# Kernel tuning notes

Measured on AMD Instinct MI355X. Metric: run time of the kernel, lower is better.

Reference implementation:

```python
import jax, jax.numpy as jnp
import numpy as np

N_VERTICES = 1_000_000
N_EDGES = 16_000_000


def setup_inputs() -> dict:
    key = jax.random.key(0)
    k1, k2, k3 = jax.random.split(key, 3)
    vertex_attr = jax.random.normal(k1, (N_VERTICES, 2), dtype=jnp.float32)
    edgeij_pair = jax.random.randint(k2, (2, N_EDGES), 0, N_VERTICES, dtype=jnp.int64)
    edge_attr = jax.random.normal(k3, (N_EDGES, 2), dtype=jnp.float32)
    g = jnp.zeros((1, 1), dtype=jnp.float32)
    batch = jnp.zeros((N_VERTICES,), dtype=jnp.int64)
    return {"vertex_attr": vertex_attr, "edgeij_pair": edgeij_pair,
            "edge_attr": edge_attr, "g": g, "batch": batch}


def reference(vertex_attr, edgeij_pair, edge_attr, g, batch):
    # c_ij: second edge feature column, [E, 1]
    c_ij = edge_attr[:, 1:2]
    b_i = vertex_attr[:, 0:1]  # [N, 1]
    x_i = vertex_attr[:, 1:2]  # [N, 1]
    n_vertices = x_i.shape[0]
    # edge-to-vertex aggregation: sum c_ij into receiving vertex i (row 0)
    cbar_i = jax.ops.segment_sum(c_ij, edgeij_pair[0], num_segments=n_vertices)
    r_i = b_i - cbar_i
    return jnp.concatenate([b_i, x_i, r_i], axis=1)  # [N, 3]
```

## Files before the change

kernel.cpp:

```cpp
#include <hip/hip_runtime.h>


#define BSHIFT 11
#define BSIZE (1 << BSHIFT)
#define NBUCK_PAD 512
#define TILE 8192
#define TPB 1024
#define PGRID 512

#define BARL() do { \
    asm volatile("s_waitcnt lgkmcnt(0)" ::: "memory"); \
    __builtin_amdgcn_s_barrier(); } while (0)

__global__ __launch_bounds__(TPB, 8)
void vu_partition(const int* __restrict__ src,
                  const float* __restrict__ eattr,
                  unsigned long long* __restrict__ pairs,
                  unsigned int* __restrict__ alloc,
                  int ne, int nbuck, int cap) {
    __shared__ unsigned long long sorted[TILE];
    __shared__ unsigned int hist[NBUCK_PAD];
    __shared__ unsigned int base_l[NBUCK_PAD];
    __shared__ unsigned int cursor[NBUCK_PAD];
    __shared__ unsigned int gbase[NBUCK_PAD];
    __shared__ unsigned int wsum[8];
    __shared__ unsigned int wexcl[8];

    const int t = threadIdx.x;
    const int nt_tiles = (ne + TILE - 1) / TILE;

    int   s0, s1, s2, s3, s4, s5, s6, s7;
    float c0, c1, c2, c3, c4, c5, c6, c7;

    int tk = blockIdx.x;

    if (tk < nt_tiles) {
        int tile0 = tk * TILE;
        if (tile0 + TILE <= ne) {
            const int* sp = src + tile0 + t;
            const float* cp = eattr + 2 * (tile0 + t) + 1;
            s0 = sp[0 * 1024]; s1 = sp[1 * 1024];
            s2 = sp[2 * 1024]; s3 = sp[3 * 1024];
            s4 = sp[4 * 1024]; s5 = sp[5 * 1024];
            s6 = sp[6 * 1024]; s7 = sp[7 * 1024];
            c0 = cp[0 * 2048]; c1 = cp[1 * 2048];
            c2 = cp[2 * 2048]; c3 = cp[3 * 2048];
            c4 = cp[4 * 2048]; c5 = cp[5 * 2048];
            c6 = cp[6 * 2048]; c7 = cp[7 * 2048];
        }
    }
    if (t < NBUCK_PAD) hist[t] = 0u;
    BARL();

    for (; tk < nt_tiles; tk += PGRID) {
        int tile0 = tk * TILE;
        int lim = ne - tile0; if (lim > TILE) lim = TILE;
        bool full = (lim == TILE);

        int nk = tk + PGRID;
        bool pv = (nk < nt_tiles) && (nk * TILE + TILE <= ne);
        int   p0s, p1s, p2s, p3s, p4s, p5s, p6s, p7s;
        float p0c, p1c, p2c, p3c, p4c, p5c, p6c, p7c;
        if (pv) {
            int ptile0 = nk * TILE;
            const int* sp = src + ptile0 + t;
            const float* cp = eattr + 2 * (ptile0 + t) + 1;
            p0s = sp[0 * 1024]; p1s = sp[1 * 1024];
            p2s = sp[2 * 1024]; p3s = sp[3 * 1024];
            p4s = sp[4 * 1024]; p5s = sp[5 * 1024];
            p6s = sp[6 * 1024]; p7s = sp[7 * 1024];
            p0c = cp[0 * 2048]; p1c = cp[1 * 2048];
            p2c = cp[2 * 2048]; p3c = cp[3 * 2048];
            p4c = cp[4 * 2048]; p5c = cp[5 * 2048];
            p6c = cp[6 * 2048]; p7c = cp[7 * 2048];
        }

        if (full) {
            atomicAdd(&hist[((unsigned)s0) >> BSHIFT], 1u);
            atomicAdd(&hist[((unsigned)s1) >> BSHIFT], 1u);
            atomicAdd(&hist[((unsigned)s2) >> BSHIFT], 1u);
            atomicAdd(&hist[((unsigned)s3) >> BSHIFT], 1u);
            atomicAdd(&hist[((unsigned)s4) >> BSHIFT], 1u);
            atomicAdd(&hist[((unsigned)s5) >> BSHIFT], 1u);
            atomicAdd(&hist[((unsigned)s6) >> BSHIFT], 1u);
            atomicAdd(&hist[((unsigned)s7) >> BSHIFT], 1u);
        } else {
            for (int i = t; i < lim; i += TPB)
                atomicAdd(&hist[((unsigned)src[tile0 + i]) >> BSHIFT], 1u);
        }
        BARL();

        unsigned int mycnt = (t < NBUCK_PAD) ? hist[t] : 0u;
        if (t < NBUCK_PAD) hist[t] = 0u;
        unsigned int gb = 0u;
        if (t < nbuck && mycnt) gb = atomicAdd(&alloc[t], mycnt);

        unsigned int x = mycnt;
        #pragma unroll
        for (int off = 1; off < 64; off <<= 1) {
            unsigned int v = __shfl_up(x, off, 64);
            if ((t & 63) >= off) x += v;
        }
        if (t < NBUCK_PAD && (t & 63) == 63) wsum[t >> 6] = x;
        BARL();
        if (t < 8) {
            unsigned int s = 0u;
            for (int k = 0; k < t; ++k) s += wsum[k];
            wexcl[t] = s;
        }
        BARL();
        if (t < NBUCK_PAD) {
            unsigned int excl = x + wexcl[t >> 6] - mycnt;
            base_l[t] = excl;
            cursor[t] = excl;
            gbase[t] = gb;
        }
        BARL();

#define VU_SCAT(sv, cv) do { \
        unsigned int q_ = ((unsigned)(sv)) >> BSHIFT; \
        unsigned int pos_ = atomicAdd(&cursor[q_], 1u); \
        sorted[pos_] = ((unsigned long long)__float_as_uint(cv) << 32) \
                       | (unsigned)(sv); } while (0)
        if (full) {
            VU_SCAT(s0, c0); VU_SCAT(s1, c1);
            VU_SCAT(s2, c2); VU_SCAT(s3, c3);
            VU_SCAT(s4, c4); VU_SCAT(s5, c5);
            VU_SCAT(s6, c6); VU_SCAT(s7, c7);
        } else {
            for (int i = t; i < lim; i += TPB) {
                int e = tile0 + i;
                int s = src[e];
                float2 ec = ((const float2*)eattr)[e];
                VU_SCAT(s, ec.y);
            }
        }
#undef VU_SCAT
        BARL();

        for (int i = t; i < lim; i += TPB) {
            unsigned long long p = sorted[i];
            unsigned int q = ((unsigned int)p) >> BSHIFT;
            unsigned int dst = q * (unsigned int)cap + gbase[q]
                             + ((unsigned int)i - base_l[q]);
            unsigned int hi = q * (unsigned int)cap + (unsigned int)cap - 1u;
            if (dst > hi) dst = hi;
            pairs[dst] = p;
        }

        s0 = p0s; s1 = p1s; s2 = p2s; s3 = p3s;
        s4 = p4s; s5 = p5s; s6 = p6s; s7 = p7s;
        c0 = p0c; c1 = p1c; c2 = p2c; c3 = p3c;
        c4 = p4c; c5 = p5c; c6 = p6c; c7 = p7c;
    }
}

__global__ __launch_bounds__(1024)
void vu_aggregate(const unsigned long long* __restrict__ pairs,
                  const unsigned int* __restrict__ alloc,
                  const float* __restrict__ vattr,
                  float* __restrict__ out,
                  int nv, int cap) {
    __shared__ float acc[BSIZE];
    __shared__ float obuf[BSIZE * 3];
    int q = blockIdx.x;
    int t = threadIdx.x;
    acc[t] = 0.0f;
    acc[t + 1024] = 0.0f;

    int v0 = q << BSHIFT;
    int iv0 = v0 + t, iv1 = v0 + t + 1024;
    float2 va0 = make_float2(0.f, 0.f), va1 = make_float2(0.f, 0.f);
    if (iv0 < nv) va0 = ((const float2*)vattr)[iv0];
    if (iv1 < nv) va1 = ((const float2*)vattr)[iv1];
    __syncthreads();

    unsigned int cnt = alloc[q];
    if (cnt > (unsigned int)cap) cnt = (unsigned int)cap;
    const unsigned long long* p = pairs + (size_t)q * (size_t)cap;
    const ulonglong2* p2 = (const ulonglong2*)p;
    unsigned int n2 = cnt >> 1;

#define VU_ACC(v64) do { \
        atomicAdd(&acc[((unsigned int)(v64)) & (BSIZE - 1)], \
                  __uint_as_float((unsigned int)((v64) >> 32))); } while (0)

    unsigned int i = t;
    for (; i + 3u * 1024u < n2; i += 4096u) {
        ulonglong2 v0 = p2[i];
        ulonglong2 v1 = p2[i + 1024u];
        ulonglong2 v2 = p2[i + 2048u];
        ulonglong2 v3 = p2[i + 3072u];
        VU_ACC(v0.x); VU_ACC(v0.y);
        VU_ACC(v1.x); VU_ACC(v1.y);
        VU_ACC(v2.x); VU_ACC(v2.y);
        VU_ACC(v3.x); VU_ACC(v3.y);
    }
    for (; i < n2; i += 1024u) {
        ulonglong2 v = p2[i];
        VU_ACC(v.x); VU_ACC(v.y);
    }
    if (t == 0 && (cnt & 1u)) {
        unsigned long long v = p[cnt - 1];
        VU_ACC(v);
    }
#undef VU_ACC
    __syncthreads();

    if (iv0 < nv) {
        obuf[3 * t + 0] = va0.x;
        obuf[3 * t + 1] = va0.y;
        obuf[3 * t + 2] = va0.x - acc[t];
    }
    {
        int i2 = t + 1024;
        if (iv1 < nv) {
            obuf[3 * i2 + 0] = va1.x;
            obuf[3 * i2 + 1] = va1.y;
            obuf[3 * i2 + 2] = va1.x - acc[i2];
        }
    }
    __syncthreads();

    long fbase = (long)q * (BSIZE * 3);
    int nfl = 3 * nv - (int)fbase;
    if (nfl > BSIZE * 3) nfl = BSIZE * 3;
    if (nfl > 0) {
        float4* o4 = (float4*)(out + fbase);
        const float4* s4 = (const float4*)obuf;
        int n4 = nfl >> 2;
        for (int j = t; j < n4; j += 1024) o4[j] = s4[j];
        for (int j = (n4 << 2) + t; j < nfl; j += 1024) out[fbase + j] = obuf[j];
    }
}

__global__ void vu_init_kernel(const float* __restrict__ vattr,
                               float* __restrict__ out, int n) {
    int i = blockIdx.x * blockDim.x + threadIdx.x;
    if (i < n) {
        float2 v = ((const float2*)vattr)[i];
        out[3 * i + 0] = v.x;
        out[3 * i + 1] = v.y;
        out[3 * i + 2] = v.x;
    }
}

__global__ void vu_scatter_kernel(const int* __restrict__ src,
                                  const float* __restrict__ eattr,
                                  float* __restrict__ out, int ne) {
    int t = blockIdx.x * blockDim.x + threadIdx.x;
    int e0 = t * 4;
    if (e0 + 3 < ne) {
        int4 idx = ((const int4*)src)[t];
        float4 a = ((const float4*)eattr)[2 * t + 0];
        float4 b = ((const float4*)eattr)[2 * t + 1];
        atomicAdd(&out[3 * idx.x + 2], -a.y);
        atomicAdd(&out[3 * idx.y + 2], -a.w);
        atomicAdd(&out[3 * idx.z + 2], -b.y);
        atomicAdd(&out[3 * idx.w + 2], -b.w);
    } else {
        for (int e = e0; e < ne; ++e)
            atomicAdd(&out[3 * src[e] + 2], -eattr[2 * e + 1]);
    }
}

extern "C" void kernel_launch(void* const* d_in, const int* in_sizes, int n_in,
                              void* d_out, int out_size, void* d_ws, size_t ws_size,
                              hipStream_t stream) {
    const float* vattr = (const float*)d_in[0];
    const int* edges = (const int*)d_in[1];
    const float* eattr = (const float*)d_in[2];
    float* out = (float*)d_out;

    int nv = in_sizes[0] / 2;
    int ne = in_sizes[2] / 2;

    int nbuck = (nv + BSIZE - 1) >> BSHIFT;
    int mean = ne / nbuck;
    int cap = mean + mean / 8 + 1024;
    cap = (cap + 15) & ~15;

    size_t alloc_bytes = 4096;
    size_t pair_bytes = (size_t)nbuck * (size_t)cap * 8ull;
    size_t need = alloc_bytes + pair_bytes;

    if (ws_size >= need && nbuck <= NBUCK_PAD) {
        unsigned int* alloc = (unsigned int*)d_ws;
        unsigned long long* pairs = (unsigned long long*)((char*)d_ws + alloc_bytes);
        (void)hipMemsetAsync(alloc, 0, (size_t)nbuck * 4, stream);

        int nt_tiles = (ne + TILE - 1) / TILE;
        int grid = PGRID; if (grid > nt_tiles) grid = nt_tiles;
        vu_partition<<<grid, TPB, 0, stream>>>(edges, eattr, pairs, alloc,
                                               ne, nbuck, cap);
        vu_aggregate<<<nbuck, 1024, 0, stream>>>(pairs, alloc, vattr, out, nv, cap);
    } else {
        int threads = 256;
        int blocks = (nv + threads - 1) / threads;
        vu_init_kernel<<<blocks, threads, 0, stream>>>(vattr, out, nv);
        int nt = (ne + 3) / 4;
        blocks = (nt + threads - 1) / threads;
        vu_scatter_kernel<<<blocks, threads, 0, stream>>>(edges, eattr, out, ne);
    }
}
```

Before: 396.9 us.

## Replicate bucket allocators per block group to cut global atomic contention

```diff
diff --git a/kernel.cpp b/kernel.cpp
--- a/kernel.cpp
+++ b/kernel.cpp
@@ -7,6 +7,7 @@
 #define TILE 8192
 #define TPB 1024
 #define PGRID 512
+#define NREP 8
 
 #define BARL() do { \
     asm volatile("s_waitcnt lgkmcnt(0)" ::: "memory"); \
@@ -17,16 +18,16 @@
                   const float* __restrict__ eattr,
                   unsigned long long* __restrict__ pairs,
                   unsigned int* __restrict__ alloc,
-                  int ne, int nbuck, int cap) {
+                  int ne, int nbuck, int cap_r) {
     __shared__ unsigned long long sorted[TILE];
     __shared__ unsigned int hist[NBUCK_PAD];
     __shared__ unsigned int base_l[NBUCK_PAD];
     __shared__ unsigned int cursor[NBUCK_PAD];
     __shared__ unsigned int gbase[NBUCK_PAD];
     __shared__ unsigned int wsum[8];
-    __shared__ unsigned int wexcl[8];
 
     const int t = threadIdx.x;
+    const int rep = blockIdx.x & (NREP - 1);
     const int nt_tiles = (ne + TILE - 1) / TILE;
 
     int   s0, s1, s2, s3, s4, s5, s6, s7;
@@ -93,7 +94,8 @@
         unsigned int mycnt = (t < NBUCK_PAD) ? hist[t] : 0u;
         if (t < NBUCK_PAD) hist[t] = 0u;
         unsigned int gb = 0u;
-        if (t < nbuck && mycnt) gb = atomicAdd(&alloc[t], mycnt);
+        if (t < nbuck && mycnt)
+            gb = atomicAdd(&alloc[rep * NBUCK_PAD + t], mycnt);
 
         unsigned int x = mycnt;
         #pragma unroll
@@ -103,14 +105,16 @@
         }
         if (t < NBUCK_PAD && (t & 63) == 63) wsum[t >> 6] = x;
         BARL();
-        if (t < 8) {
-            unsigned int s = 0u;
-            for (int k = 0; k < t; ++k) s += wsum[k];
-            wexcl[t] = s;
-        }
-        BARL();
+
+        unsigned int wx = 0u;
+        int wid = t >> 6;
+        #pragma unroll
+        for (int k = 0; k < 7; ++k) {
+            unsigned int w = wsum[k];
+            if (k < wid) wx += w;
+        }
         if (t < NBUCK_PAD) {
-            unsigned int excl = x + wexcl[t >> 6] - mycnt;
+            unsigned int excl = x + wx - mycnt;
             base_l[t] = excl;
             cursor[t] = excl;
             gbase[t] = gb;
@@ -141,9 +145,10 @@
         for (int i = t; i < lim; i += TPB) {
             unsigned long long p = sorted[i];
             unsigned int q = ((unsigned int)p) >> BSHIFT;
-            unsigned int dst = q * (unsigned int)cap + gbase[q]
+            unsigned int seg = (q << 3) + (unsigned int)rep;
+            unsigned int dst = seg * (unsigned int)cap_r + gbase[q]
                              + ((unsigned int)i - base_l[q]);
-            unsigned int hi = q * (unsigned int)cap + (unsigned int)cap - 1u;
+            unsigned int hi = seg * (unsigned int)cap_r + (unsigned int)cap_r - 1u;
             if (dst > hi) dst = hi;
             pairs[dst] = p;
         }
@@ -160,7 +165,7 @@
                   const unsigned int* __restrict__ alloc,
                   const float* __restrict__ vattr,
                   float* __restrict__ out,
-                  int nv, int cap) {
+                  int nv, int cap_r) {
     __shared__ float acc[BSIZE];
     __shared__ float obuf[BSIZE * 3];
     int q = blockIdx.x;
@@ -173,36 +178,34 @@
     float2 va0 = make_float2(0.f, 0.f), va1 = make_float2(0.f, 0.f);
     if (iv0 < nv) va0 = ((const float2*)vattr)[iv0];
     if (iv1 < nv) va1 = ((const float2*)vattr)[iv1];
+
+    unsigned int cnts[NREP];
+    #pragma unroll
+    for (int r = 0; r < NREP; ++r) {
+        unsigned int c = alloc[r * NBUCK_PAD + q];
+        cnts[r] = (c > (unsigned int)cap_r) ? (unsigned int)cap_r : c;
+    }
     __syncthreads();
-
-    unsigned int cnt = alloc[q];
-    if (cnt > (unsigned int)cap) cnt = (unsigned int)cap;
-    const unsigned long long* p = pairs + (size_t)q * (size_t)cap;
-    const ulonglong2* p2 = (const ulonglong2*)p;
-    unsigned int n2 = cnt >> 1;
 
 #define VU_ACC(v64) do { \
         atomicAdd(&acc[((unsigned int)(v64)) & (BSIZE - 1)], \
                   __uint_as_float((unsigned int)((v64) >> 32))); } while (0)
 
-    unsigned int i = t;
-    for (; i + 3u * 1024u < n2; i += 4096u) {
-        ulonglong2 v0 = p2[i];
-        ulonglong2 v1 = p2[i + 1024u];
-        ulonglong2 v2 = p2[i + 2048u];
-        ulonglong2 v3 = p2[i + 3072u];
-        VU_ACC(v0.x); VU_ACC(v0.y);
-        VU_ACC(v1.x); VU_ACC(v1.y);
-        VU_ACC(v2.x); VU_ACC(v2.y);
-        VU_ACC(v3.x); VU_ACC(v3.y);
-    }
-    for (; i < n2; i += 1024u) {
-        ulonglong2 v = p2[i];
-        VU_ACC(v.x); VU_ACC(v.y);
-    }
-    if (t == 0 && (cnt & 1u)) {
-        unsigned long long v = p[cnt - 1];
-        VU_ACC(v);
+    #pragma unroll
+    for (int r = 0; r < NREP; ++r) {
+        unsigned int cnt = cnts[r];
+        const unsigned long long* p =
+            pairs + (size_t)(q * NREP + r) * (size_t)cap_r;
+        const ulonglong2* p2 = (const ulonglong2*)p;
+        unsigned int n2 = cnt >> 1;
+        for (unsigned int i = t; i < n2; i += 1024u) {
+            ulonglong2 v = p2[i];
+            VU_ACC(v.x); VU_ACC(v.y);
+        }
+        if (t == 0 && (cnt & 1u)) {
+            unsigned long long v = p[cnt - 1];
+            VU_ACC(v);
+        }
     }
 #undef VU_ACC
     __syncthreads();
@@ -276,24 +279,25 @@
     int ne = in_sizes[2] / 2;
 
     int nbuck = (nv + BSIZE - 1) >> BSHIFT;
-    int mean = ne / nbuck;
-    int cap = mean + mean / 8 + 1024;
-    cap = (cap + 15) & ~15;
-
-    size_t alloc_bytes = 4096;
-    size_t pair_bytes = (size_t)nbuck * (size_t)cap * 8ull;
+    int mean_r = ne / nbuck / NREP;
+    int cap_r = mean_r + mean_r / 8;
+    cap_r = (cap_r + 15) & ~15;
+
+    size_t alloc_bytes = (size_t)NREP * NBUCK_PAD * 4;
+    size_t pair_bytes = (size_t)nbuck * NREP * (size_t)cap_r * 8ull;
     size_t need = alloc_bytes + pair_bytes;
 
     if (ws_size >= need && nbuck <= NBUCK_PAD) {
         unsigned int* alloc = (unsigned int*)d_ws;
         unsigned long long* pairs = (unsigned long long*)((char*)d_ws + alloc_bytes);
-        (void)hipMemsetAsync(alloc, 0, (size_t)nbuck * 4, stream);
+        (void)hipMemsetAsync(alloc, 0, alloc_bytes, stream);
 
         int nt_tiles = (ne + TILE - 1) / TILE;
         int grid = PGRID; if (grid > nt_tiles) grid = nt_tiles;
         vu_partition<<<grid, TPB, 0, stream>>>(edges, eattr, pairs, alloc,
-                                               ne, nbuck, cap);
-        vu_aggregate<<<nbuck, 1024, 0, stream>>>(pairs, alloc, vattr, out, nv, cap);
+                                               ne, nbuck, cap_r);
+        vu_aggregate<<<nbuck, 1024, 0, stream>>>(pairs, alloc, vattr, out,
+                                                 nv, cap_r);
     } else {
         int threads = 256;
         int blocks = (nv + threads - 1) / threads;
```

Result: faster. 373.3 us (-5.9%).
